# Kernel optimization log

Measured on AMD Instinct MI355X. Metric: run time of the kernel, lower is better.

## Reference

```python
import jax, jax.numpy as jnp
import numpy as np
import math

HEAD_DIM = 128
LAMBDA_INIT = 0.8
GN_EPS = 1e-05
NEG = -1e9


def ghostmax(scores):
    # softmax with an extra implicit zero logit (softmax-plus-one)
    m = jnp.maximum(jnp.max(scores, axis=-1, keepdims=True), 0.0)
    e = jnp.exp(scores - m)
    return e / (jnp.sum(e, axis=-1, keepdims=True) + jnp.exp(-m))


def setup_inputs() -> dict:
    key = jax.random.key(0)
    ks = jax.random.split(key, 8)
    B, H2, H, S, D = 2, 16, 8, 2048, HEAD_DIM
    return {
        "q": jax.random.normal(ks[0], (B, H2, S, D), dtype=jnp.float32),
        "k": jax.random.normal(ks[1], (B, H2, S, D), dtype=jnp.float32),
        "v": jax.random.normal(ks[2], (B, H, S, D), dtype=jnp.float32),
        "lambda_q1": 0.1 * jax.random.normal(ks[3], (D,), dtype=jnp.float32),
        "lambda_k1": 0.1 * jax.random.normal(ks[4], (D,), dtype=jnp.float32),
        "lambda_q2": 0.1 * jax.random.normal(ks[5], (D,), dtype=jnp.float32),
        "lambda_k2": 0.1 * jax.random.normal(ks[6], (D,), dtype=jnp.float32),
        "gn_weight": jnp.ones((H * D,), dtype=jnp.float32),
        "gn_bias": jnp.zeros((H * D,), dtype=jnp.float32),
    }


def reference(q, k, v, lambda_q1, lambda_k1, lambda_q2, lambda_k2, gn_weight, gn_bias):
    B, H2, S, D = q.shape
    H = H2 // 2
    scaling = 1.0 / math.sqrt(D)
    # [B, 2H, S, S] attention scores
    scores = jnp.einsum("bhsd,bhtd->bhst", q, k) * scaling
    causal_mask = jnp.triu(jnp.full((S, S), NEG, dtype=scores.dtype), k=1)
    scores = scores + causal_mask[None, None]
    w = ghostmax(scores)
    w = w.reshape(B, H, 2, S, S)
    lam = (
        jnp.exp(jnp.sum(lambda_q1 * lambda_k1))
        - jnp.exp(jnp.sum(lambda_q2 * lambda_k2))
        + LAMBDA_INIT
    )
    w = w[:, :, 0] - lam * w[:, :, 1]  # [B, H, S, S]
    out = jnp.einsum("bhst,bhtd->bhsd", w, v)  # [B, H, S, D]
    # torch .reshape(B, -1, S): raw row-major reinterpretation
    out = out.reshape(B, H * D, S)
    # GroupNorm: num_groups=H over channels H*D, normalized over (group channels, seq)
    g = out.reshape(B, H, D * S)
    mean = jnp.mean(g, axis=-1, keepdims=True)
    var = jnp.var(g, axis=-1, keepdims=True)
    g = (g - mean) * jax.lax.rsqrt(var + GN_EPS)
    out = g.reshape(B, H * D, S) * gn_weight[None, :, None] + gn_bias[None, :, None]
    return out * (1.0 - LAMBDA_INIT)
```

## Files before the change

kernel.cpp:

```cpp
#include <hip/hip_runtime.h>
#include <hip/hip_bf16.h>
#include <cstddef>
#include <cstdint>


typedef __bf16 bf16x8 __attribute__((ext_vector_type(8)));
typedef __bf16 bf16x4 __attribute__((ext_vector_type(4)));
typedef float f32x4 __attribute__((ext_vector_type(4)));

constexpr int SEQ = 2048;
constexpr int DH  = 128;
constexpr int NH  = 8;
constexpr int NH2 = 16;
constexpr float SCALE = 0.088388347648318447f;

constexpr size_t QK_ELEMS = (size_t)2 * NH2 * SEQ * DH;
constexpr size_t V_ELEMS  = (size_t)2 * NH  * SEQ * DH;
constexpr size_t OFF_KB   = 4096;
constexpr size_t OFF_VT   = OFF_KB + QK_ELEMS * 2;
constexpr size_t WS_NEED  = OFF_VT + V_ELEMS * 2;

__device__ __forceinline__ void load_lds16(const void* g, void* l) {
  __builtin_amdgcn_global_load_lds(
      (const __attribute__((address_space(1))) uint32_t*)g,
      (__attribute__((address_space(3))) uint32_t*)l, 16, 0, 0);
}

__device__ __forceinline__ bf16x8 cvt8(float4 a, float4 b) {
  bf16x8 r;
  r[0] = (__bf16)a.x; r[1] = (__bf16)a.y; r[2] = (__bf16)a.z; r[3] = (__bf16)a.w;
  r[4] = (__bf16)b.x; r[5] = (__bf16)b.y; r[6] = (__bf16)b.z; r[7] = (__bf16)b.w;
  return r;
}

__global__ __launch_bounds__(256) void cvt_kernel(
    const float* __restrict__ in, __bf16* __restrict__ out)
{
  const size_t i = ((size_t)blockIdx.x * 256 + threadIdx.x) * 8;
  float4 a = *(const float4*)(in + i);
  float4 b = *(const float4*)(in + i + 4);
  *(bf16x8*)(out + i) = cvt8(a, b);
}

__global__ __launch_bounds__(256) void vt_kernel(
    const float* __restrict__ v, __bf16* __restrict__ vt)
{
  __shared__ float tile[32][33];
  const int tt = blockIdx.x, dt = blockIdx.y, bh = blockIdx.z;
  const int tr = threadIdx.x >> 3, tc = (threadIdx.x & 7) * 4;
  const float* src = v + ((size_t)bh * SEQ + tt * 32) * DH + dt * 32;
  float4 f = *(const float4*)(src + (size_t)tr * DH + tc);
  tile[tr][tc + 0] = f.x; tile[tr][tc + 1] = f.y;
  tile[tr][tc + 2] = f.z; tile[tr][tc + 3] = f.w;
  __syncthreads();
  __bf16* dst = vt + ((size_t)bh * DH + dt * 32 + tr) * SEQ + tt * 32 + tc;
  bf16x4 o;
  o[0] = (__bf16)tile[tc + 0][tr];
  o[1] = (__bf16)tile[tc + 1][tr];
  o[2] = (__bf16)tile[tc + 2][tr];
  o[3] = (__bf16)tile[tc + 3][tr];
  *(bf16x4*)dst = o;
}

__global__ __launch_bounds__(256, 2) void attn2_kernel(
    const float* __restrict__ Qf, const __bf16* __restrict__ Kb,
    const __bf16* __restrict__ Vtb,
    const float* __restrict__ lq1, const float* __restrict__ lk1,
    const float* __restrict__ lq2, const float* __restrict__ lk2,
    float* __restrict__ Obuf, float* __restrict__ stats)
{
  __shared__ __align__(16) __bf16 ldsK[2][2][32][128];
  __shared__ __align__(16) __bf16 ldsVt[2][128][32];
  __shared__ __align__(16) __bf16 ldsP[4][2][16][40];

  const int qt = 31 - blockIdx.x;
  const int bh = blockIdx.y;
  const int b = bh >> 3, h = bh & 7;
  const int tid = threadIdx.x;
  const int w = tid >> 6, lane = tid & 63;
  const int l15 = lane & 15, quad = lane >> 4;

  float a1 = lq1[lane]*lk1[lane] + lq1[lane+64]*lk1[lane+64];
  float a2 = lq2[lane]*lk2[lane] + lq2[lane+64]*lk2[lane+64];
  #pragma unroll
  for (int off = 1; off < 64; off <<= 1) {
    a1 += __shfl_xor(a1, off);
    a2 += __shfl_xor(a2, off);
  }
  const float lam = __expf(a1) - __expf(a2) + 0.8f;

  const size_t headQK = (size_t)(b*NH2 + 2*h) * SEQ * DH;
  const float*  Qh  = Qf + headQK;
  const __bf16* Kh  = Kb + headQK;
  const __bf16* Vth = Vtb + (size_t)(b*NH + h) * DH * SEQ;

  size_t goffK[4];
  #pragma unroll
  for (int i = 0; i < 4; ++i) {
    const int R  = w*16 + i*4 + quad;
    const int sh = R >> 5, kr = R & 31;
    const int cs = lane & 15;
    goffK[i] = ((size_t)sh * SEQ + kr) * DH + ((cs ^ (kr & 15)) * 8);
  }
  size_t goffV[2];
  #pragma unroll
  for (int i = 0; i < 2; ++i) {
    const int d  = w*32 + i*16 + (lane >> 2);
    const int cs = lane & 3;
    goffV[i] = (size_t)d * SEQ + ((cs ^ (d & 3)) * 8);
  }

  __bf16* ldsKb0 = &ldsK[0][0][0][0];
  __bf16* ldsVb0 = &ldsVt[0][0][0];

  const int qb = qt * 64, nsteps = 2 * (qt + 1);

  const int qrow = qb + w*16 + l15;
  bf16x8 qf[2][4];
  #pragma unroll
  for (int sh = 0; sh < 2; ++sh) {
    const float* src = Qh + (size_t)sh*SEQ*DH + (size_t)qrow*DH + quad*8;
    #pragma unroll
    for (int kd = 0; kd < 4; ++kd) {
      float4 f0 = *(const float4*)(src + kd*32);
      float4 f1 = *(const float4*)(src + kd*32 + 4);
      f0.x *= SCALE; f0.y *= SCALE; f0.z *= SCALE; f0.w *= SCALE;
      f1.x *= SCALE; f1.y *= SCALE; f1.z *= SCALE; f1.w *= SCALE;
      qf[sh][kd] = cvt8(f0, f1);
    }
  }

  f32x4 oacc[2][8];
  float lsum[2][4];
  #pragma unroll
  for (int sh = 0; sh < 2; ++sh) {
    #pragma unroll
    for (int nt = 0; nt < 8; ++nt) oacc[sh][nt] = (f32x4){0.f,0.f,0.f,0.f};
    #pragma unroll
    for (int r = 0; r < 4; ++r) lsum[sh][r] = 0.f;
  }

  {
    const __bf16* kg = Kh;
    #pragma unroll
    for (int i = 0; i < 4; ++i)
      load_lds16(kg + goffK[i], ldsKb0 + w*2048 + i*512);
    const __bf16* vg = Vth;
    #pragma unroll
    for (int i = 0; i < 2; ++i)
      load_lds16(vg + goffV[i], ldsVb0 + w*1024 + i*512);
  }
  __syncthreads();

  for (int st = 0; st < nsteps; ++st) {
    const int cur = st & 1;
    const int kbt = st * 32;

    if (st + 1 < nsteps) {
      const int nxt = cur ^ 1;
      const __bf16* kg = Kh + (size_t)(kbt + 32) * DH;
      #pragma unroll
      for (int i = 0; i < 4; ++i)
        load_lds16(kg + goffK[i], ldsKb0 + (size_t)nxt*8192 + w*2048 + i*512);
      const __bf16* vg = Vth + (kbt + 32);
      #pragma unroll
      for (int i = 0; i < 2; ++i)
        load_lds16(vg + goffV[i], ldsVb0 + (size_t)nxt*4096 + w*1024 + i*512);
    }

    f32x4 sacc[2][2];
    #pragma unroll
    for (int sh = 0; sh < 2; ++sh)
      #pragma unroll
      for (int n = 0; n < 2; ++n)
        sacc[sh][n] = (f32x4){0.f,0.f,0.f,0.f};
    #pragma unroll
    for (int sh = 0; sh < 2; ++sh)
      #pragma unroll
      for (int n = 0; n < 2; ++n)
        #pragma unroll
        for (int kd = 0; kd < 4; ++kd) {
          bf16x8 kf = *(const bf16x8*)&ldsK[cur][sh][n*16 + l15][((kd*4 + quad) ^ l15) * 8];
          sacc[sh][n] = __builtin_amdgcn_mfma_f32_16x16x32_bf16(qf[sh][kd], kf, sacc[sh][n], 0, 0, 0);
        }

    const int qrow0 = qb + w*16 + quad*4;
    #pragma unroll
    for (int sh = 0; sh < 2; ++sh)
      #pragma unroll
      for (int r = 0; r < 4; ++r) {
        const int qr = qrow0 + r;
        const float p0 = (kbt + l15      <= qr) ? __expf(sacc[sh][0][r]) : 0.f;
        const float p1 = (kbt + l15 + 16 <= qr) ? __expf(sacc[sh][1][r]) : 0.f;
        lsum[sh][r] += p0 + p1;
        ldsP[w][sh][quad*4 + r][l15]      = (__bf16)p0;
        ldsP[w][sh][quad*4 + r][l15 + 16] = (__bf16)p1;
      }

    {
      bf16x8 pf0 = *(const bf16x8*)&ldsP[w][0][l15][quad*8];
      bf16x8 pf1 = *(const bf16x8*)&ldsP[w][1][l15][quad*8];
      #pragma unroll
      for (int nt = 0; nt < 8; ++nt) {
        bf16x8 vf = *(const bf16x8*)&ldsVt[cur][nt*16 + l15][(quad ^ (l15 & 3)) * 8];
        oacc[0][nt] = __builtin_amdgcn_mfma_f32_16x16x32_bf16(pf0, vf, oacc[0][nt], 0, 0, 0);
        oacc[1][nt] = __builtin_amdgcn_mfma_f32_16x16x32_bf16(pf1, vf, oacc[1][nt], 0, 0, 0);
      }
    }
    __syncthreads();
  }

  #pragma unroll
  for (int sh = 0; sh < 2; ++sh)
    #pragma unroll
    for (int r = 0; r < 4; ++r) {
      float vsum = lsum[sh][r];
      #pragma unroll
      for (int off = 1; off < 16; off <<= 1) vsum += __shfl_xor(vsum, off);
      lsum[sh][r] = vsum + 1.0f;
    }

  const int qrow0 = qb + w*16 + quad*4;
  float* obase = Obuf + (size_t)(b*NH + h) * SEQ * DH;
  float sum = 0.f, ss = 0.f;
  #pragma unroll
  for (int r = 0; r < 4; ++r) {
    const float i0 = 1.0f / lsum[0][r];
    const float i1 = lam / lsum[1][r];
    float* orow = obase + (size_t)(qrow0 + r) * DH + l15;
    #pragma unroll
    for (int nt = 0; nt < 8; ++nt) {
      const float val = oacc[0][nt][r] * i0 - oacc[1][nt][r] * i1;
      orow[nt*16] = val;
      sum += val;
      ss  += val * val;
    }
  }
  #pragma unroll
  for (int off = 1; off < 64; off <<= 1) {
    sum += __shfl_xor(sum, off);
    ss  += __shfl_xor(ss, off);
  }
  if (lane == 0) {
    atomicAdd(&stats[2*(b*NH + h)],     sum);
    atomicAdd(&stats[2*(b*NH + h) + 1], ss);
  }
}

__global__ __launch_bounds__(256) void attn_fb_kernel(
    const float* __restrict__ q, const float* __restrict__ k,
    const float* __restrict__ v,
    const float* __restrict__ lq1, const float* __restrict__ lk1,
    const float* __restrict__ lq2, const float* __restrict__ lk2,
    float* __restrict__ Obuf, float* __restrict__ stats)
{
  __shared__ __align__(16) __bf16 lds_k[2][32][136];
  __shared__ __align__(16) __bf16 lds_vt[128][40];
  __shared__ __align__(16) __bf16 lds_p[4][2][16][40];

  const int qt = blockIdx.x, h = blockIdx.y, b = blockIdx.z;
  const int qb = qt * 64;
  const int tid = threadIdx.x;
  const int w = tid >> 6, lane = tid & 63;
  const int l15 = lane & 15, quad = lane >> 4;

  float a1 = lq1[lane]*lk1[lane] + lq1[lane+64]*lk1[lane+64];
  float a2 = lq2[lane]*lk2[lane] + lq2[lane+64]*lk2[lane+64];
  #pragma unroll
  for (int off = 1; off < 64; off <<= 1) {
    a1 += __shfl_xor(a1, off);
    a2 += __shfl_xor(a2, off);
  }
  const float lam = __expf(a1) - __expf(a2) + 0.8f;

  const float* qh0 = q + (size_t)(b*NH2 + 2*h) * SEQ * DH;
  const float* qh1 = qh0 + (size_t)SEQ * DH;
  const float* kh0 = k + (size_t)(b*NH2 + 2*h) * SEQ * DH;
  const float* kh1 = kh0 + (size_t)SEQ * DH;
  const float* vh  = v + (size_t)(b*NH + h) * SEQ * DH;

  bf16x8 qf[2][4];
  {
    const int qrow = qb + w*16 + l15;
    #pragma unroll
    for (int sh = 0; sh < 2; ++sh) {
      const float* src = (sh ? qh1 : qh0) + (size_t)qrow * DH + quad*8;
      #pragma unroll
      for (int kd = 0; kd < 4; ++kd) {
        float4 f0 = *(const float4*)(src + kd*32);
        float4 f1 = *(const float4*)(src + kd*32 + 4);
        qf[sh][kd] = cvt8(f0, f1);
      }
    }
  }

  f32x4 oacc[2][8];
  #pragma unroll
  for (int sh = 0; sh < 2; ++sh)
    #pragma unroll
    for (int nt = 0; nt < 8; ++nt)
      oacc[sh][nt] = (f32x4){0.f,0.f,0.f,0.f};

  float mst[2][4] = {{0.f,0.f,0.f,0.f},{0.f,0.f,0.f,0.f}};
  float lst[2][4] = {{1.f,1.f,1.f,1.f},{1.f,1.f,1.f,1.f}};

  const int krow = tid >> 2, ksh = krow >> 5, kr = krow & 31;
  const int kd0 = (tid & 3) * 32;
  const float* ksrc0 = (ksh ? kh1 : kh0) + kd0;
  const int vt = tid >> 3, vd = (tid & 7) * 16;

  const int nsteps = (qb + 64) / 32;
  for (int st = 0; st < nsteps; ++st) {
    const int kbt = st * 32;
    {
      const float* sp = ksrc0 + (size_t)(kbt + kr) * DH;
      #pragma unroll
      for (int c = 0; c < 4; ++c) {
        float4 f0 = *(const float4*)(sp + c*8);
        float4 f1 = *(const float4*)(sp + c*8 + 4);
        *(bf16x8*)&lds_k[ksh][kr][kd0 + c*8] = cvt8(f0, f1);
      }
      const float* vp = vh + (size_t)(kbt + vt) * DH + vd;
      #pragma unroll
      for (int c = 0; c < 4; ++c) {
        float4 f = *(const float4*)(vp + c*4);
        lds_vt[vd + c*4 + 0][vt] = (__bf16)f.x;
        lds_vt[vd + c*4 + 1][vt] = (__bf16)f.y;
        lds_vt[vd + c*4 + 2][vt] = (__bf16)f.z;
        lds_vt[vd + c*4 + 3][vt] = (__bf16)f.w;
      }
    }
    __syncthreads();

    f32x4 sacc[2][2];
    #pragma unroll
    for (int sh = 0; sh < 2; ++sh)
      #pragma unroll
      for (int n = 0; n < 2; ++n)
        sacc[sh][n] = (f32x4){0.f,0.f,0.f,0.f};

    #pragma unroll
    for (int sh = 0; sh < 2; ++sh)
      #pragma unroll
      for (int n = 0; n < 2; ++n)
        #pragma unroll
        for (int kd = 0; kd < 4; ++kd) {
          bf16x8 bf = *(const bf16x8*)&lds_k[sh][n*16 + l15][kd*32 + quad*8];
          sacc[sh][n] = __builtin_amdgcn_mfma_f32_16x16x32_bf16(qf[sh][kd], bf, sacc[sh][n], 0, 0, 0);
        }

    const int qrow0 = qb + w*16 + quad*4;
    const int c0 = kbt + l15, c1 = c0 + 16;
    #pragma unroll
    for (int sh = 0; sh < 2; ++sh) {
      #pragma unroll
      for (int r = 0; r < 4; ++r) {
        float s0 = sacc[sh][0][r] * SCALE;
        float s1 = sacc[sh][1][r] * SCALE;
        const int qr = qrow0 + r;
        if (c0 > qr) s0 = -1e30f;
        if (c1 > qr) s1 = -1e30f;
        float mx = fmaxf(s0, s1);
        #pragma unroll
        for (int off = 1; off < 16; off <<= 1)
          mx = fmaxf(mx, __shfl_xor(mx, off));
        const float mnew = fmaxf(mst[sh][r], mx);
        const float alpha = __expf(mst[sh][r] - mnew);
        mst[sh][r] = mnew;
        const float p0 = __expf(s0 - mnew);
        const float p1 = __expf(s1 - mnew);
        float rs = p0 + p1;
        #pragma unroll
        for (int off = 1; off < 16; off <<= 1)
          rs += __shfl_xor(rs, off);
        lst[sh][r] = lst[sh][r] * alpha + rs;
        #pragma unroll
        for (int nt = 0; nt < 8; ++nt)
          oacc[sh][nt][r] *= alpha;
        lds_p[w][sh][quad*4 + r][l15]      = (__bf16)p0;
        lds_p[w][sh][quad*4 + r][l15 + 16] = (__bf16)p1;
      }
    }

    {
      bf16x8 pf0 = *(const bf16x8*)&lds_p[w][0][l15][quad*8];
      bf16x8 pf1 = *(const bf16x8*)&lds_p[w][1][l15][quad*8];
      #pragma unroll
      for (int nt = 0; nt < 8; ++nt) {
        bf16x8 vf = *(const bf16x8*)&lds_vt[nt*16 + l15][quad*8];
        oacc[0][nt] = __builtin_amdgcn_mfma_f32_16x16x32_bf16(pf0, vf, oacc[0][nt], 0, 0, 0);
        oacc[1][nt] = __builtin_amdgcn_mfma_f32_16x16x32_bf16(pf1, vf, oacc[1][nt], 0, 0, 0);
      }
    }
    __syncthreads();
  }

  const int qrow0 = qb + w*16 + quad*4;
  float* obase = Obuf + (size_t)(b*NH + h) * SEQ * DH;
  float sum = 0.f, ss = 0.f;
  #pragma unroll
  for (int r = 0; r < 4; ++r) {
    const float i0 = 1.0f / lst[0][r];
    const float i1 = lam / lst[1][r];
    float* orow = obase + (size_t)(qrow0 + r) * DH + l15;
    #pragma unroll
    for (int nt = 0; nt < 8; ++nt) {
      const float val = oacc[0][nt][r] * i0 - oacc[1][nt][r] * i1;
      orow[nt*16] = val;
      sum += val;
      ss  += val * val;
    }
  }
  #pragma unroll
  for (int off = 1; off < 64; off <<= 1) {
    sum += __shfl_xor(sum, off);
    ss  += __shfl_xor(ss, off);
  }
  if (lane == 0) {
    atomicAdd(&stats[2*(b*NH + h)],     sum);
    atomicAdd(&stats[2*(b*NH + h) + 1], ss);
  }
}

__global__ __launch_bounds__(256) void norm_kernel(
    float* __restrict__ Obuf, const float* __restrict__ stats,
    const float* __restrict__ gw, const float* __restrict__ gb)
{
  const int idx = (blockIdx.x * 256 + threadIdx.x) * 4;
  const int bh = idx >> 18;
  const int local = idx & 262143;
  const float inv = 1.0f / 262144.0f;
  const float mean = stats[2*bh] * inv;
  const float var  = stats[2*bh + 1] * inv - mean * mean;
  const float rstd = rsqrtf(var + 1e-5f);
  const int c = ((bh & 7) << 7) + (local >> 11);
  const float wq = gw[c] * rstd;
  const float bq = gb[c];
  float4 o = *(const float4*)(Obuf + idx);
  float4 r;
  r.x = ((o.x - mean) * wq + bq) * 0.2f;
  r.y = ((o.y - mean) * wq + bq) * 0.2f;
  r.z = ((o.z - mean) * wq + bq) * 0.2f;
  r.w = ((o.w - mean) * wq + bq) * 0.2f;
  *(float4*)(Obuf + idx) = r;
}

extern "C" void kernel_launch(void* const* d_in, const int* in_sizes, int n_in,
                              void* d_out, int out_size, void* d_ws, size_t ws_size,
                              hipStream_t stream) {
  const float* q   = (const float*)d_in[0];
  const float* k   = (const float*)d_in[1];
  const float* v   = (const float*)d_in[2];
  const float* lq1 = (const float*)d_in[3];
  const float* lk1 = (const float*)d_in[4];
  const float* lq2 = (const float*)d_in[5];
  const float* lk2 = (const float*)d_in[6];
  const float* gw  = (const float*)d_in[7];
  const float* gb  = (const float*)d_in[8];
  float* out = (float*)d_out;
  float* stats = (float*)d_ws;

  (void)hipMemsetAsync(d_ws, 0, 256, stream);

  if (ws_size >= WS_NEED) {
    __bf16* Kb  = (__bf16*)((char*)d_ws + OFF_KB);
    __bf16* Vtb = (__bf16*)((char*)d_ws + OFF_VT);

    cvt_kernel<<<QK_ELEMS / 2048, 256, 0, stream>>>(k, Kb);
    vt_kernel<<<dim3(64, 4, 16), 256, 0, stream>>>(v, Vtb);

    attn2_kernel<<<dim3(32, 16), 256, 0, stream>>>(q, Kb, Vtb,
        lq1, lk1, lq2, lk2, out, stats);
  } else {
    attn_fb_kernel<<<dim3(32, NH, 2), 256, 0, stream>>>(q, k, v,
        lq1, lk1, lq2, lk2, out, stats);
  }

  const int total = 2 * NH * SEQ * DH;
  norm_kernel<<<total / 1024, 256, 0, stream>>>(out, stats, gw, gb);
}
```

Measured before the change: 232.3 us.

## Fuse K conversion, V transpose and stats zeroing into one prep kernel

The separate K-to-bf16 conversion kernel, V transpose kernel and the workspace memset are merged into a single prep launch. Block IDs select which job each block does, and block 0 zeroes the stats. The change removes two launches and the gaps between them. The attention kernel also reverses its query-tile order for the second half of heads, so the long causal tiles for those heads are no longer all scheduled first, which is meant to balance load across CUs.

```diff
diff --git a/kernel.cpp b/kernel.cpp
--- a/kernel.cpp
+++ b/kernel.cpp
@@ -33,33 +33,36 @@
   return r;
 }
 
-__global__ __launch_bounds__(256) void cvt_kernel(
-    const float* __restrict__ in, __bf16* __restrict__ out)
-{
-  const size_t i = ((size_t)blockIdx.x * 256 + threadIdx.x) * 8;
-  float4 a = *(const float4*)(in + i);
-  float4 b = *(const float4*)(in + i + 4);
-  *(bf16x8*)(out + i) = cvt8(a, b);
-}
-
-__global__ __launch_bounds__(256) void vt_kernel(
-    const float* __restrict__ v, __bf16* __restrict__ vt)
+__global__ __launch_bounds__(256) void prep_kernel(
+    const float* __restrict__ k, const float* __restrict__ v,
+    __bf16* __restrict__ Kb, __bf16* __restrict__ Vtb,
+    float* __restrict__ stats)
 {
   __shared__ float tile[32][33];
-  const int tt = blockIdx.x, dt = blockIdx.y, bh = blockIdx.z;
-  const int tr = threadIdx.x >> 3, tc = (threadIdx.x & 7) * 4;
-  const float* src = v + ((size_t)bh * SEQ + tt * 32) * DH + dt * 32;
-  float4 f = *(const float4*)(src + (size_t)tr * DH + tc);
-  tile[tr][tc + 0] = f.x; tile[tr][tc + 1] = f.y;
-  tile[tr][tc + 2] = f.z; tile[tr][tc + 3] = f.w;
-  __syncthreads();
-  __bf16* dst = vt + ((size_t)bh * DH + dt * 32 + tr) * SEQ + tt * 32 + tc;
-  bf16x4 o;
-  o[0] = (__bf16)tile[tc + 0][tr];
-  o[1] = (__bf16)tile[tc + 1][tr];
-  o[2] = (__bf16)tile[tc + 2][tr];
-  o[3] = (__bf16)tile[tc + 3][tr];
-  *(bf16x4*)dst = o;
+  const int id = blockIdx.x;
+  if (id == 0 && threadIdx.x < 64) stats[threadIdx.x] = 0.f;
+  if (id < 4096) {
+    const size_t i = ((size_t)id * 256 + threadIdx.x) * 8;
+    float4 a = *(const float4*)(k + i);
+    float4 b = *(const float4*)(k + i + 4);
+    *(bf16x8*)(Kb + i) = cvt8(a, b);
+  } else {
+    const int vid = id - 4096;
+    const int tt = vid & 63, dt = (vid >> 6) & 3, bh = vid >> 8;
+    const int tr = threadIdx.x >> 3, tc = (threadIdx.x & 7) * 4;
+    const float* src = v + ((size_t)bh * SEQ + tt * 32) * DH + dt * 32;
+    float4 f = *(const float4*)(src + (size_t)tr * DH + tc);
+    tile[tr][tc + 0] = f.x; tile[tr][tc + 1] = f.y;
+    tile[tr][tc + 2] = f.z; tile[tr][tc + 3] = f.w;
+    __syncthreads();
+    __bf16* dst = Vtb + ((size_t)bh * DH + dt * 32 + tr) * SEQ + tt * 32 + tc;
+    bf16x4 o;
+    o[0] = (__bf16)tile[tc + 0][tr];
+    o[1] = (__bf16)tile[tc + 1][tr];
+    o[2] = (__bf16)tile[tc + 2][tr];
+    o[3] = (__bf16)tile[tc + 3][tr];
+    *(bf16x4*)dst = o;
+  }
 }
 
 __global__ __launch_bounds__(256, 2) void attn2_kernel(
@@ -73,7 +76,7 @@
   __shared__ __align__(16) __bf16 ldsVt[2][128][32];
   __shared__ __align__(16) __bf16 ldsP[4][2][16][40];
 
-  const int qt = 31 - blockIdx.x;
+  const int qt = (blockIdx.y < 8) ? (31 - (int)blockIdx.x) : (int)blockIdx.x;
   const int bh = blockIdx.y;
   const int b = bh >> 3, h = bh & 7;
   const int tid = threadIdx.x;
@@ -460,18 +463,16 @@
   float* out = (float*)d_out;
   float* stats = (float*)d_ws;
 
-  (void)hipMemsetAsync(d_ws, 0, 256, stream);
-
   if (ws_size >= WS_NEED) {
     __bf16* Kb  = (__bf16*)((char*)d_ws + OFF_KB);
     __bf16* Vtb = (__bf16*)((char*)d_ws + OFF_VT);
 
-    cvt_kernel<<<QK_ELEMS / 2048, 256, 0, stream>>>(k, Kb);
-    vt_kernel<<<dim3(64, 4, 16), 256, 0, stream>>>(v, Vtb);
+    prep_kernel<<<8192, 256, 0, stream>>>(k, v, Kb, Vtb, stats);
 
     attn2_kernel<<<dim3(32, 16), 256, 0, stream>>>(q, Kb, Vtb,
         lq1, lk1, lq2, lk2, out, stats);
   } else {
+    (void)hipMemsetAsync(d_ws, 0, 256, stream);
     attn_fb_kernel<<<dim3(32, NH, 2), 256, 0, stream>>>(q, k, v,
         lq1, lk1, lq2, lk2, out, stats);
   }
```

Measured after the change: 216.5 us. -6.8%, faster.
